# Kernel optimization log

Measured on AMD Instinct MI355X. Metric: run time of the kernel, lower is better.

The kernel has to match this reference:

```python
import jax, jax.numpy as jnp
import numpy as np

B, S, D, N = 8, 4096, 768, 64


def setup_inputs() -> dict:
    key = jax.random.key(0)
    k1, k2 = jax.random.split(key)
    word_vectors = jax.random.normal(k1, (B, S, D), dtype=jnp.float32)
    sent_rep_token_ids = jnp.sort(jax.random.randint(k2, (B, N), 0, S), axis=1)
    sent_rep_mask = jnp.ones((B, N), dtype=jnp.float32)
    # sent_lengths: each row must sum exactly to S (torch.split contract).
    rng = np.random.default_rng(0)
    lens = np.stack([
        np.diff(np.concatenate([[0], np.sort(rng.choice(np.arange(1, S), N - 1, replace=False)), [S]]))
        for _ in range(B)
    ])
    sent_lengths = jnp.asarray(lens, dtype=jnp.int64) if jax.config.jax_enable_x64 else jnp.asarray(lens, dtype=jnp.int32)
    sent_lengths_mask = jnp.ones((B, N), dtype=jnp.float32)
    return {
        "word_vectors": word_vectors,
        "sent_rep_token_ids": sent_rep_token_ids,
        "sent_rep_mask": sent_rep_mask,
        "sent_lengths": sent_lengths,
        "sent_lengths_mask": sent_lengths_mask,
    }


def reference(word_vectors, sent_rep_token_ids, sent_rep_mask, sent_lengths, sent_lengths_mask):
    b, s, d = word_vectors.shape
    n = sent_lengths.shape[1]
    dt = word_vectors.dtype

    # --- sent_rep_tokens branch: gather CLS-style token per sentence ---
    rep_vec = jnp.take_along_axis(word_vectors, sent_rep_token_ids[:, :, None], axis=1)  # [B,N,D]
    rep_vec = rep_vec * sent_rep_mask[:, :, None].astype(dt)

    # --- mean_tokens branch: ragged per-segment mean via segment_sum ---
    ends = jnp.cumsum(sent_lengths, axis=1)                      # [B,N] exclusive-end offsets
    pos = jnp.arange(s)
    seg = jax.vmap(lambda e: jnp.searchsorted(e, pos, side='right'))(ends)  # [B,S] segment id per token
    gseg = (seg + jnp.arange(b)[:, None] * n).reshape(-1)        # global segment ids [B*S]
    flat = word_vectors.reshape(b * s, d)
    sums = jax.ops.segment_sum(flat, gseg, num_segments=b * n).reshape(b, n, d)
    counts = jax.ops.segment_sum((flat != 0).astype(dt), gseg, num_segments=b * n).reshape(b, n, d)
    mean = sums / jnp.maximum(counts, 1)
    # fallback to word_vectors[0,0] when a segment has zero nonzero entries (original semantics)
    all_zero = (counts.sum(axis=-1) == 0)                        # [B,N]
    mean = jnp.where(all_zero[:, :, None], word_vectors[0, 0], mean)
    mean_vec = mean * sent_lengths_mask[:, :, None].astype(dt)

    out_vectors = jnp.concatenate([rep_vec, mean_vec], axis=1)   # [B,2N,D]
    out_masks = jnp.concatenate([sent_rep_mask, sent_lengths_mask], axis=1)  # [B,2N]
    return out_vectors, out_masks
```

## Files before the change

### kernel.cpp

```cpp
#include <hip/hip_runtime.h>

#define BB 8
#define SS 4096
#define DD 768
#define NN 64
#define D4 (DD / 4)
#define CHT 128
#define MAXCH 96
#define NREC (BB * MAXCH)

typedef float nfloat4 __attribute__((ext_vector_type(4)));

__global__ __launch_bounds__(256, 8) void chunk_kernel(
    const float* __restrict__ wv,
    const int* __restrict__ lens,
    float* __restrict__ ws_sum,
    unsigned char* __restrict__ ws_cnt)
{
    const int cidx = blockIdx.x / 3;
    const int g    = blockIdx.x % 3;
    const int b    = blockIdx.y;
    const int tid  = threadIdx.x;
    const int lane = tid & 63;
    const int w    = tid >> 6;

    const int l    = lens[b * NN + lane];
    const int nchl = (l + CHT - 1) >> 7;
    int inclen = l, inch = nchl;
    #pragma unroll
    for (int off = 1; off < 64; off <<= 1) {
        int a = __shfl_up(inclen, off); if (lane >= off) inclen += a;
        int c = __shfl_up(inch,   off); if (lane >= off) inch   += c;
    }
    const int total_ch = __shfl(inch, 63);
    if (cidx >= total_ch) return;

    unsigned long long m = __ballot(inch > cidx);
    const int n         = __ffsll(m) - 1;
    const int seg_len   = __shfl(l, n);
    const int seg_start = __shfl(inclen, n) - seg_len;
    const int ch_base   = __shfl(inch, n) - __shfl(nchl, n);
    const int t0 = seg_start + (cidx - ch_base) * CHT;
    const int t1 = min(seg_start + seg_len, t0 + CHT);

    const int col4 = g * 64 + lane;
    const nfloat4* base = (const nfloat4*)wv + (size_t)b * SS * D4 + col4;

    float4 s = make_float4(0.f, 0.f, 0.f, 0.f);
    float4 c = make_float4(0.f, 0.f, 0.f, 0.f);
    #pragma unroll 8
    for (int t = t0 + w; t < t1; t += 4) {
        nfloat4 v = __builtin_nontemporal_load(base + (size_t)t * D4);
        s.x += v.x; s.y += v.y; s.z += v.z; s.w += v.w;
        c.x += (v.x != 0.f) ? 1.f : 0.f;
        c.y += (v.y != 0.f) ? 1.f : 0.f;
        c.z += (v.z != 0.f) ? 1.f : 0.f;
        c.w += (v.w != 0.f) ? 1.f : 0.f;
    }

    __shared__ float4 s_s[4][64];
    __shared__ float4 s_c[4][64];
    s_s[w][lane] = s;
    s_c[w][lane] = c;
    __syncthreads();

    if (tid < 64) {
        float4 S = make_float4(0.f, 0.f, 0.f, 0.f);
        float4 C = make_float4(0.f, 0.f, 0.f, 0.f);
        #pragma unroll
        for (int j = 0; j < 4; ++j) {
            float4 a = s_s[j][tid], d = s_c[j][tid];
            S.x += a.x; S.y += a.y; S.z += a.z; S.w += a.w;
            C.x += d.x; C.y += d.y; C.z += d.z; C.w += d.w;
        }
        const size_t rec = (size_t)(b * MAXCH + cidx);
        ((float4*)ws_sum)[rec * D4 + g * 64 + tid] = S;
        uchar4 u;
        u.x = (unsigned char)C.x; u.y = (unsigned char)C.y;
        u.z = (unsigned char)C.z; u.w = (unsigned char)C.w;
        ((uchar4*)ws_cnt)[rec * D4 + g * 64 + tid] = u;
    }
}

__global__ __launch_bounds__(256) void finalize_kernel(
    const float* __restrict__ wv,
    const int* __restrict__ rep_ids,
    const float* __restrict__ rep_mask,
    const int* __restrict__ lens,
    const float* __restrict__ len_mask,
    const float* __restrict__ ws_sum,
    const unsigned char* __restrict__ ws_cnt,
    float* __restrict__ out)
{
    __shared__ float s_part[4];
    __shared__ int s_info[2];
    const int sgid = blockIdx.x;
    const int b = sgid >> 6, n = sgid & 63;
    const int tid = threadIdx.x;
    const int lane = tid & 63;

    if (tid < 64) {
        const int l    = lens[b * NN + tid];
        const int nchl = (l + CHT - 1) >> 7;
        int inch = nchl;
        #pragma unroll
        for (int off = 1; off < 64; off <<= 1) {
            int a = __shfl_up(inch, off); if (lane >= off) inch += a;
        }
        if (tid == n) { s_info[0] = inch - nchl; s_info[1] = nchl; }
    }
    __syncthreads();
    const int ch_base = s_info[0];
    const int K       = s_info[1];
    const bool active = tid < D4;

    float4 S = make_float4(0,0,0,0), C = S;
    if (active) {
        for (int k = 0; k < K; ++k) {
            const size_t rec = (size_t)(b * MAXCH + ch_base + k);
            float4 sv = ((const float4*)ws_sum)[rec * D4 + tid];
            uchar4 cv = ((const uchar4*)ws_cnt)[rec * D4 + tid];
            S.x += sv.x; S.y += sv.y; S.z += sv.z; S.w += sv.w;
            C.x += (float)cv.x; C.y += (float)cv.y;
            C.z += (float)cv.z; C.w += (float)cv.w;
        }
    }

    float tot = C.x + C.y + C.z + C.w;
    #pragma unroll
    for (int off = 32; off; off >>= 1) tot += __shfl_xor(tot, off);
    if ((tid & 63) == 0) s_part[tid >> 6] = tot;
    __syncthreads();
    const float total = s_part[0] + s_part[1] + s_part[2] + s_part[3];

    if (active) {
        float4 mean;
        mean.x = S.x / fmaxf(C.x, 1.f);
        mean.y = S.y / fmaxf(C.y, 1.f);
        mean.z = S.z / fmaxf(C.z, 1.f);
        mean.w = S.w / fmaxf(C.w, 1.f);
        if (total == 0.f) mean = ((const float4*)wv)[tid];

        const float lm = len_mask[sgid];
        mean.x *= lm; mean.y *= lm; mean.z *= lm; mean.w *= lm;

        float4* out4 = (float4*)out;
        out4[(size_t)(b * 2 * NN + NN + n) * D4 + tid] = mean;

        const int   rid = rep_ids[sgid];
        const float rm  = rep_mask[sgid];
        float4 rv = ((const float4*)wv)[(size_t)(b * SS + rid) * D4 + tid];
        rv.x *= rm; rv.y *= rm; rv.z *= rm; rv.w *= rm;
        out4[(size_t)(b * 2 * NN + n) * D4 + tid] = rv;

        if (tid == 0) {
            float* masks = out + (size_t)BB * 2 * NN * DD;
            masks[b * 2 * NN + n]      = rm;
            masks[b * 2 * NN + NN + n] = lm;
        }
    }
}

extern "C" void kernel_launch(void* const* d_in, const int* in_sizes, int n_in,
                              void* d_out, int out_size, void* d_ws, size_t ws_size,
                              hipStream_t stream) {
    const float* wv       = (const float*)d_in[0];
    const int*   rep_ids  = (const int*)d_in[1];
    const float* rep_mask = (const float*)d_in[2];
    const int*   lens     = (const int*)d_in[3];
    const float* len_mask = (const float*)d_in[4];
    float*       out      = (float*)d_out;
    float*         ws_sum = (float*)d_ws;
    unsigned char* ws_cnt = (unsigned char*)d_ws + (size_t)NREC * DD * 4;

    dim3 gridB(3 * MAXCH, BB);
    chunk_kernel<<<gridB, 256, 0, stream>>>(wv, lens, ws_sum, ws_cnt);
    finalize_kernel<<<BB * NN, 256, 0, stream>>>(wv, rep_ids, rep_mask, lens,
                                                 len_mask, ws_sum, ws_cnt, out);
}
```

Before: 158.1 us.

## Fuse chunk reduction and finalize into one kernel via last-block atomic counter

Merges the chunk partial-sum kernel and the finalize kernel into a single launch. Each segment gets an atomic counter; the last of its 3*K contributing blocks, detected after a threadfence, reduces the workspace partials and writes the mean, rep-token and mask outputs. This removes the second kernel launch and the idle gap between kernels, at the cost of a memset for the counters, extra atomics and fences, and a serialized tail in the last block per segment. Launch bounds are relaxed from (256,8) to 256.

```diff
diff --git a/kernel.cpp b/kernel.cpp
--- a/kernel.cpp
+++ b/kernel.cpp
@@ -8,14 +8,23 @@
 #define CHT 128
 #define MAXCH 96
 #define NREC (BB * MAXCH)
+#define SUM_BYTES ((size_t)NREC * DD * 4)
+#define CNT_BYTES ((size_t)NREC * DD)
+#define CTR_OFF   (SUM_BYTES + CNT_BYTES)
+#define CTR_BYTES (BB * NN * 4)
 
 typedef float nfloat4 __attribute__((ext_vector_type(4)));
 
-__global__ __launch_bounds__(256, 8) void chunk_kernel(
+__global__ __launch_bounds__(256) void fused_kernel(
     const float* __restrict__ wv,
+    const int* __restrict__ rep_ids,
+    const float* __restrict__ rep_mask,
     const int* __restrict__ lens,
+    const float* __restrict__ len_mask,
     float* __restrict__ ws_sum,
-    unsigned char* __restrict__ ws_cnt)
+    unsigned char* __restrict__ ws_cnt,
+    int* __restrict__ ctr,
+    float* __restrict__ out)
 {
     const int cidx = blockIdx.x / 3;
     const int g    = blockIdx.x % 3;
@@ -39,7 +48,8 @@
     const int n         = __ffsll(m) - 1;
     const int seg_len   = __shfl(l, n);
     const int seg_start = __shfl(inclen, n) - seg_len;
-    const int ch_base   = __shfl(inch, n) - __shfl(nchl, n);
+    const int K         = __shfl(nchl, n);
+    const int ch_base   = __shfl(inch, n) - K;
     const int t0 = seg_start + (cidx - ch_base) * CHT;
     const int t1 = min(seg_start + seg_len, t0 + CHT);
 
@@ -60,6 +70,8 @@
 
     __shared__ float4 s_s[4][64];
     __shared__ float4 s_c[4][64];
+    __shared__ float s_part[4];
+    __shared__ int s_last;
     s_s[w][lane] = s;
     s_c[w][lane] = c;
     __syncthreads();
@@ -80,38 +92,19 @@
         u.z = (unsigned char)C.z; u.w = (unsigned char)C.w;
         ((uchar4*)ws_cnt)[rec * D4 + g * 64 + tid] = u;
     }
-}
 
-__global__ __launch_bounds__(256) void finalize_kernel(
-    const float* __restrict__ wv,
-    const int* __restrict__ rep_ids,
-    const float* __restrict__ rep_mask,
-    const int* __restrict__ lens,
-    const float* __restrict__ len_mask,
-    const float* __restrict__ ws_sum,
-    const unsigned char* __restrict__ ws_cnt,
-    float* __restrict__ out)
-{
-    __shared__ float s_part[4];
-    __shared__ int s_info[2];
-    const int sgid = blockIdx.x;
-    const int b = sgid >> 6, n = sgid & 63;
-    const int tid = threadIdx.x;
-    const int lane = tid & 63;
-
-    if (tid < 64) {
-        const int l    = lens[b * NN + tid];
-        const int nchl = (l + CHT - 1) >> 7;
-        int inch = nchl;
-        #pragma unroll
-        for (int off = 1; off < 64; off <<= 1) {
-            int a = __shfl_up(inch, off); if (lane >= off) inch += a;
-        }
-        if (tid == n) { s_info[0] = inch - nchl; s_info[1] = nchl; }
+    __syncthreads();
+    if (tid == 0) {
+        __threadfence();
+        int old = atomicAdd(&ctr[b * NN + n], 1);
+        s_last = (old == 3 * K - 1);
     }
     __syncthreads();
-    const int ch_base = s_info[0];
-    const int K       = s_info[1];
+    if (!s_last) return;
+
+    __threadfence();
+
+    const int sgid = b * NN + n;
     const bool active = tid < D4;
 
     float4 S = make_float4(0,0,0,0), C = S;
@@ -171,10 +164,10 @@
     const float* len_mask = (const float*)d_in[4];
     float*       out      = (float*)d_out;
     float*         ws_sum = (float*)d_ws;
-    unsigned char* ws_cnt = (unsigned char*)d_ws + (size_t)NREC * DD * 4;
+    unsigned char* ws_cnt = (unsigned char*)d_ws + SUM_BYTES;
+    int*           ctr    = (int*)((char*)d_ws + CTR_OFF);
 
-    dim3 gridB(3 * MAXCH, BB);
-    chunk_kernel<<<gridB, 256, 0, stream>>>(wv, lens, ws_sum, ws_cnt);
-    finalize_kernel<<<BB * NN, 256, 0, stream>>>(wv, rep_ids, rep_mask, lens,
-                                                 len_mask, ws_sum, ws_cnt, out);
+    hipMemsetAsync(ctr, 0, CTR_BYTES, stream);
+    fused_kernel<<<dim3(3 * MAXCH, BB), 256, 0, stream>>>(
+        wv, rep_ids, rep_mask, lens, len_mask, ws_sum, ws_cnt, ctr, out);
 }
```

After: 370.7 us. 2.34x slower.
